# Kernel optimization log

Hardware: AMD Instinct MI355X
Metric: run time of the kernel (lower is better)

The kernel has to match this reference:

```python
import jax, jax.numpy as jnp
import numpy as np

DIM = 513          # SSP dimension (odd)
N_PARAM = (DIM - 1) // 2
BATCH = 131072


def setup_inputs() -> dict:
    key = jax.random.key(0)
    k1, k2 = jax.random.split(key)
    inputs = jax.random.normal(k1, (BATCH, 1), dtype=jnp.float32)
    # phis initialized uniform in (-pi+0.001, pi-0.001) like the torch module
    phis = jax.random.uniform(k2, (N_PARAM,), dtype=jnp.float32,
                              minval=-np.pi + 0.001, maxval=np.pi - 0.001)
    return {"inputs": inputs, "phis": phis}


def reference(inputs, phis):
    # uf is unit-modulus with conjugate-symmetric spectrum:
    #   uf[0] = 1, uf[1:h] = exp(i*phis), uf[-1:dim//2:-1] = conj(exp(i*phis))
    # so angle(uf) = [0, phis, -phis[::-1]] and uf**x = exp(i * x * angles).
    zero = jnp.zeros((1,), dtype=phis.dtype)
    angles = jnp.concatenate([zero, phis, -phis[::-1]])      # (dim,)
    # inputs: (B, 1) broadcasts against angles (dim,) -> (B, dim)
    spectrum = jnp.exp(1j * (inputs * angles[None, :]).astype(jnp.float32))
    out = jnp.fft.ifft(spectrum, axis=-1).real               # (B, dim)
    return out
```

## Files before the change

kernel.cpp:

```cpp
#include <hip/hip_runtime.h>


#define DIMN 513
#define KDIM 512
#define NPAD 544
#define NPAIRS 17
#define BM 128
#define INV_N (1.0f / 513.0f)

typedef __attribute__((ext_vector_type(8))) short short8;
typedef __attribute__((ext_vector_type(4))) float f32x4;
typedef __attribute__((ext_vector_type(4))) float f4;

__device__ __forceinline__ short bf16r(float f) {
  unsigned u = __float_as_uint(f);
  u += 0x7FFFu + ((u >> 16) & 1u);
  return (short)(u >> 16);
}

__global__ void ssp_genB(unsigned short* __restrict__ bt) {
  int idx = blockIdx.x * 256 + threadIdx.x;
  int n = idx >> 9;
  int k = idx & 511;
  int j = k & 255;
  unsigned prod = (unsigned)(j + 1) * (unsigned)n;
  unsigned m = prod % 513u;
  float ang = (float)m * (6.283185307179586f / 513.0f);
  float s, c;
  __sincosf(ang, &s, &c);
  float v = (k < 256) ? c * (2.0f / 513.0f) : -(s * (2.0f / 513.0f));
  unsigned chunk = (unsigned)n >> 5;
  unsigned w = ((unsigned)(n & 31) << 10) + ((unsigned)k << 1);
  unsigned phys = (chunk << 15) + (w ^ ((unsigned)(n & 7) << 4));
  bt[phys >> 1] = (unsigned short)bf16r(v);
}

__global__ __launch_bounds__(256, 2) void ssp_main(
    const float* __restrict__ x, const float* __restrict__ phis,
    const unsigned short* __restrict__ bt, float* __restrict__ out) {
  __shared__ __align__(16) unsigned char lds[65536];
  const int tid = threadIdx.x;
  const int w = tid >> 6;
  const int lane = tid & 63;
  const int r = lane & 15;
  const int q = lane >> 4;
  const long rowW = (long)blockIdx.x * BM + w * 32;

  short8 afrag[2][16];
  const float x0 = x[rowW + r];
  const float x1 = x[rowW + 16 + r];
#pragma unroll
  for (int u = 0; u < 8; ++u) {
    const f4* pp4 = (const f4*)(phis + 32 * u + 8 * q);
    f4 plo = pp4[0];
    f4 phi4 = pp4[1];
#pragma unroll
    for (int e = 0; e < 8; ++e) {
      float ph = (e < 4) ? plo[e] : phi4[e - 4];
      float s0, c0, s1, c1;
      __sincosf(x0 * ph, &s0, &c0);
      __sincosf(x1 * ph, &s1, &c1);
      afrag[0][u][e]     = bf16r(c0);
      afrag[0][u + 8][e] = bf16r(s0);
      afrag[1][u][e]     = bf16r(c1);
      afrag[1][u + 8][e] = bf16r(s1);
    }
  }

  const unsigned char* btb = (const unsigned char*)bt;

  {
    const unsigned char* src = btb + (w * 8) * 1024 + lane * 16;
    unsigned char* dst = &lds[(w * 8) * 1024];
#pragma unroll
    for (int i = 0; i < 8; ++i)
      __builtin_amdgcn_global_load_lds(
          (const __attribute__((address_space(1))) unsigned int*)(src + i * 1024),
          (__attribute__((address_space(3))) unsigned int*)(dst + i * 1024),
          16, 0, 0);
  }
  __syncthreads();

  const int sw  = (r & 7) << 4;
  const int be0 = (r << 10)        + ((q << 4) ^ sw);
  const int bo0 = (r << 10)        + ((64 | (q << 4)) ^ sw);
  const int be1 = ((16 + r) << 10) + ((q << 4) ^ sw);
  const int bo1 = ((16 + r) << 10) + ((64 | (q << 4)) ^ sw);

  const long outRowBase = rowW + 4 * q;

  for (int p = 0; p < NPAIRS; ++p) {
    const int buf = (p & 1) * 32768;

    if (p + 1 < NPAIRS) {
      const unsigned char* src = btb + (p + 1) * 32768 + (w * 8) * 1024 + lane * 16;
      unsigned char* dst = &lds[((p + 1) & 1) * 32768 + (w * 8) * 1024];
#pragma unroll
      for (int i = 0; i < 8; ++i)
        __builtin_amdgcn_global_load_lds(
            (const __attribute__((address_space(1))) unsigned int*)(src + i * 1024),
            (__attribute__((address_space(3))) unsigned int*)(dst + i * 1024),
            16, 0, 0);
    }

    f32x4 acc00 = {0.f, 0.f, 0.f, 0.f};
    f32x4 acc01 = {0.f, 0.f, 0.f, 0.f};
    f32x4 acc10 = {0.f, 0.f, 0.f, 0.f};
    f32x4 acc11 = {0.f, 0.f, 0.f, 0.f};
#pragma unroll
    for (int t = 0; t < 16; ++t) {
      const int o0 = buf + ((t & 1) ? bo0 : be0) + (t >> 1) * 128;
      const int o1 = buf + ((t & 1) ? bo1 : be1) + (t >> 1) * 128;
      short8 b0 = *(const short8*)&lds[o0];
      short8 b1 = *(const short8*)&lds[o1];
      acc00 = __builtin_amdgcn_mfma_f32_16x16x32_bf16(afrag[0][t], b0, acc00, 0, 0, 0);
      acc10 = __builtin_amdgcn_mfma_f32_16x16x32_bf16(afrag[1][t], b0, acc10, 0, 0, 0);
      acc01 = __builtin_amdgcn_mfma_f32_16x16x32_bf16(afrag[0][t], b1, acc01, 0, 0, 0);
      acc11 = __builtin_amdgcn_mfma_f32_16x16x32_bf16(afrag[1][t], b1, acc11, 0, 0, 0);
    }

    const int col0 = p * 32 + r;
#pragma unroll
    for (int rr = 0; rr < 4; ++rr) {
      const long ro0 = (outRowBase + rr) * DIMN;
      const long ro1 = (outRowBase + 16 + rr) * DIMN;
      if (col0 < DIMN) {
        out[ro0 + col0] = acc00[rr] + INV_N;
        out[ro1 + col0] = acc10[rr] + INV_N;
      }
      if (col0 + 16 < DIMN) {
        out[ro0 + col0 + 16] = acc01[rr] + INV_N;
        out[ro1 + col0 + 16] = acc11[rr] + INV_N;
      }
    }

    __syncthreads();
  }
}

extern "C" void kernel_launch(void* const* d_in, const int* in_sizes, int n_in,
                              void* d_out, int out_size, void* d_ws, size_t ws_size,
                              hipStream_t stream) {
  const float* x = (const float*)d_in[0];
  const float* phis = (const float*)d_in[1];
  float* out = (float*)d_out;
  unsigned short* bt = (unsigned short*)d_ws;

  ssp_genB<<<dim3(NPAD * KDIM / 256), dim3(256), 0, stream>>>(bt);
  ssp_main<<<dim3(131072 / BM), dim3(256), 0, stream>>>(x, phis, bt, out);
}
```

Measured before the change: 361.7 us.

## Transpose MFMA output for vector row stores and relax per-iteration waits

Swaps the MFMA A/B operands so each lane holds four consecutive output columns of one row. Each lane can then write a 16-byte unaligned vector store instead of four scalar stores, with the odd last column handled separately. The first basis-tile global-to-LDS load is now issued before the sincos fragment generation so it overlaps that compute. The per-iteration __syncthreads is replaced by a partial vmcnt wait plus s_barrier, so in-flight output stores no longer block the loop; this relies on in-order vmcnt accounting to guarantee the prefetched tile has landed.

```diff
diff --git a/kernel.cpp b/kernel.cpp
--- a/kernel.cpp
+++ b/kernel.cpp
@@ -11,6 +11,7 @@
 typedef __attribute__((ext_vector_type(8))) short short8;
 typedef __attribute__((ext_vector_type(4))) float f32x4;
 typedef __attribute__((ext_vector_type(4))) float f4;
+typedef __attribute__((ext_vector_type(4), aligned(4))) float f4u;
 
 __device__ __forceinline__ short bf16r(float f) {
   unsigned u = __float_as_uint(f);
@@ -46,6 +47,19 @@
   const int q = lane >> 4;
   const long rowW = (long)blockIdx.x * BM + w * 32;
 
+  const unsigned char* btb = (const unsigned char*)bt;
+
+  {
+    const unsigned char* src = btb + (w * 8) * 1024 + lane * 16;
+    unsigned char* dst = &lds[(w * 8) * 1024];
+#pragma unroll
+    for (int i = 0; i < 8; ++i)
+      __builtin_amdgcn_global_load_lds(
+          (const __attribute__((address_space(1))) unsigned int*)(src + i * 1024),
+          (__attribute__((address_space(3))) unsigned int*)(dst + i * 1024),
+          16, 0, 0);
+  }
+
   short8 afrag[2][16];
   const float x0 = x[rowW + r];
   const float x1 = x[rowW + 16 + r];
@@ -67,19 +81,8 @@
     }
   }
 
-  const unsigned char* btb = (const unsigned char*)bt;
-
-  {
-    const unsigned char* src = btb + (w * 8) * 1024 + lane * 16;
-    unsigned char* dst = &lds[(w * 8) * 1024];
-#pragma unroll
-    for (int i = 0; i < 8; ++i)
-      __builtin_amdgcn_global_load_lds(
-          (const __attribute__((address_space(1))) unsigned int*)(src + i * 1024),
-          (__attribute__((address_space(3))) unsigned int*)(dst + i * 1024),
-          16, 0, 0);
-  }
-  __syncthreads();
+  asm volatile("s_waitcnt vmcnt(0) lgkmcnt(0)" ::: "memory");
+  __builtin_amdgcn_s_barrier();
 
   const int sw  = (r & 7) << 4;
   const int be0 = (r << 10)        + ((q << 4) ^ sw);
@@ -87,7 +90,8 @@
   const int be1 = ((16 + r) << 10) + ((q << 4) ^ sw);
   const int bo1 = ((16 + r) << 10) + ((64 | (q << 4)) ^ sw);
 
-  const long outRowBase = rowW + 4 * q;
+  float* const o0 = out + (rowW + r) * DIMN;
+  float* const o1 = out + (rowW + 16 + r) * DIMN;
 
   for (int p = 0; p < NPAIRS; ++p) {
     const int buf = (p & 1) * 32768;
@@ -102,6 +106,7 @@
             (__attribute__((address_space(3))) unsigned int*)(dst + i * 1024),
             16, 0, 0);
     }
+    __builtin_amdgcn_sched_barrier(0);
 
     f32x4 acc00 = {0.f, 0.f, 0.f, 0.f};
     f32x4 acc01 = {0.f, 0.f, 0.f, 0.f};
@@ -109,32 +114,32 @@
     f32x4 acc11 = {0.f, 0.f, 0.f, 0.f};
 #pragma unroll
     for (int t = 0; t < 16; ++t) {
-      const int o0 = buf + ((t & 1) ? bo0 : be0) + (t >> 1) * 128;
-      const int o1 = buf + ((t & 1) ? bo1 : be1) + (t >> 1) * 128;
-      short8 b0 = *(const short8*)&lds[o0];
-      short8 b1 = *(const short8*)&lds[o1];
-      acc00 = __builtin_amdgcn_mfma_f32_16x16x32_bf16(afrag[0][t], b0, acc00, 0, 0, 0);
-      acc10 = __builtin_amdgcn_mfma_f32_16x16x32_bf16(afrag[1][t], b0, acc10, 0, 0, 0);
-      acc01 = __builtin_amdgcn_mfma_f32_16x16x32_bf16(afrag[0][t], b1, acc01, 0, 0, 0);
-      acc11 = __builtin_amdgcn_mfma_f32_16x16x32_bf16(afrag[1][t], b1, acc11, 0, 0, 0);
+      const int o0b = buf + ((t & 1) ? bo0 : be0) + (t >> 1) * 128;
+      const int o1b = buf + ((t & 1) ? bo1 : be1) + (t >> 1) * 128;
+      short8 b0 = *(const short8*)&lds[o0b];
+      short8 b1 = *(const short8*)&lds[o1b];
+      acc00 = __builtin_amdgcn_mfma_f32_16x16x32_bf16(b0, afrag[0][t], acc00, 0, 0, 0);
+      acc10 = __builtin_amdgcn_mfma_f32_16x16x32_bf16(b0, afrag[1][t], acc10, 0, 0, 0);
+      acc01 = __builtin_amdgcn_mfma_f32_16x16x32_bf16(b1, afrag[0][t], acc01, 0, 0, 0);
+      acc11 = __builtin_amdgcn_mfma_f32_16x16x32_bf16(b1, afrag[1][t], acc11, 0, 0, 0);
     }
 
-    const int col0 = p * 32 + r;
-#pragma unroll
-    for (int rr = 0; rr < 4; ++rr) {
-      const long ro0 = (outRowBase + rr) * DIMN;
-      const long ro1 = (outRowBase + 16 + rr) * DIMN;
-      if (col0 < DIMN) {
-        out[ro0 + col0] = acc00[rr] + INV_N;
-        out[ro1 + col0] = acc10[rr] + INV_N;
-      }
-      if (col0 + 16 < DIMN) {
-        out[ro0 + col0 + 16] = acc01[rr] + INV_N;
-        out[ro1 + col0 + 16] = acc11[rr] + INV_N;
+    const int nb = p * 32 + 4 * q;
+    if (p < 16) {
+      *(f4u*)(o0 + nb)      = acc00 + INV_N;
+      *(f4u*)(o0 + nb + 16) = acc01 + INV_N;
+      *(f4u*)(o1 + nb)      = acc10 + INV_N;
+      *(f4u*)(o1 + nb + 16) = acc11 + INV_N;
+    } else {
+      if (q == 0) {
+        o0[512] = acc00[0] + INV_N;
+        o1[512] = acc10[0] + INV_N;
       }
     }
+    __builtin_amdgcn_sched_barrier(0);
 
-    __syncthreads();
+    asm volatile("s_waitcnt vmcnt(4)" ::: "memory");
+    __builtin_amdgcn_s_barrier();
   }
 }
 
```

Measured after the change: 354.2 us. 2.1% less time.
